# Performance work log

Measured on AMD Instinct MI355X. Metric: run time of the kernel, lower is better.

## Reference

```python
import jax, jax.numpy as jnp
import numpy as np

B, T, D, H = 128, 512, 64, 256  # batch, n_target, input_size, hidden_size

def setup_inputs() -> dict:
    key = jax.random.key(0)
    ks = jax.random.split(key, 12)
    sc_ih = 1.0 / np.sqrt(H)
    return {
        "x_input": jax.random.normal(ks[0], (B, T * D), dtype=jnp.float32),
        "h0": jax.random.normal(ks[1], (1, B, H), dtype=jnp.float32) * 0.1,
        "c0": jax.random.normal(ks[2], (1, B, H), dtype=jnp.float32) * 0.1,
        "W_ih": jax.random.normal(ks[3], (4 * H, D), dtype=jnp.float32) * sc_ih,
        "W_hh": jax.random.normal(ks[4], (4 * H, H), dtype=jnp.float32) * sc_ih,
        "b_ih": jax.random.normal(ks[5], (4 * H,), dtype=jnp.float32) * sc_ih,
        "b_hh": jax.random.normal(ks[6], (4 * H,), dtype=jnp.float32) * sc_ih,
        "f1_w": jax.random.normal(ks[7], (128, H), dtype=jnp.float32) * sc_ih,
        "f1_b": jax.random.normal(ks[8], (128,), dtype=jnp.float32) * sc_ih,
        "f2_w": jax.random.normal(ks[9], (128, H), dtype=jnp.float32) * sc_ih,
        "f2_b": jax.random.normal(ks[10], (128,), dtype=jnp.float32) * sc_ih,
        "long": 10,
    }

def reference(x_input, h0, c0, W_ih, W_hh, b_ih, b_hh, f1_w, f1_b, f2_w, f2_b, long):
    b = x_input.shape[0]
    d = W_ih.shape[1]
    state = x_input.reshape(b, -1, d)            # (B, T, D)
    t = state.shape[1]
    h_prev, c_prev = h0[0], c0[0]                # (B, H) shared initial state for every step
    # All single-step LSTM calls are independent -> one batched GEMM over (B, T)
    gates = (jnp.einsum('btd,gd->btg', state, W_ih) + b_ih
             + (h_prev @ W_hh.T + b_hh)[:, None, :])         # (B, T, 4H)
    i_g, f_g, g_g, o_g = jnp.split(gates, 4, axis=-1)        # torch gate order: i, f, g, o
    i_g = jax.nn.sigmoid(i_g); f_g = jax.nn.sigmoid(f_g)
    g_g = jnp.tanh(g_g);       o_g = jax.nn.sigmoid(o_g)
    c_all = f_g * c_prev[:, None, :] + i_g * g_g             # (B, T, H)
    h_all = o_g * jnp.tanh(c_all)
    # original loop starts at i=1, so step 0 keeps zero hidden/cell
    mask = (jnp.arange(t) > 0).astype(x_input.dtype)[None, :, None]
    h_all = h_all * mask
    c_all = c_all * mask
    w0 = state[:, :, 0] / long                               # (B, T)
    w1 = state[:, :, 1]
    def agg(v):
        a = jnp.einsum('bth,kh->btk', v, f1_w) + f1_b        # f1 per step
        bb = jnp.einsum('bth,kh->btk', v, f2_w) + f2_b       # f2 per step
        first = jnp.einsum('btk,bt->bk', a, w0)              # weighted sum over t
        second = jnp.einsum('btk,bt->bk', bb, w1)
        return jnp.concatenate([first, second], axis=-1)[None]  # (1, B, 256)
    return (agg(h_all), agg(c_all))
```

## Files before the change

### kernel.cpp

```cpp
#include <hip/hip_runtime.h>

#define BDIM 128
#define TDIM 512
#define DDIM 64
#define HDIM 256
#define BH   (BDIM * HDIM)
#define HH_OFF (4 * BH)

typedef short s16x8 __attribute__((ext_vector_type(8)));
typedef float f32x4 __attribute__((ext_vector_type(4)));

#if __has_builtin(__builtin_amdgcn_exp2f)
#define EXP2(x) __builtin_amdgcn_exp2f(x)
#else
#define EXP2(x) exp2f(x)
#endif
#define L2E 1.44269504f

__device__ __forceinline__ float rcpf(float x) { return __builtin_amdgcn_rcpf(x); }

__device__ __forceinline__ short f2bf(float f) {
  __bf16 b = (__bf16)f;
  return __builtin_bit_cast(short, b);
}

__device__ __forceinline__ s16x8 pack_bf8(float4 lo, float4 hi) {
  s16x8 v;
  v[0] = f2bf(lo.x); v[1] = f2bf(lo.y); v[2] = f2bf(lo.z); v[3] = f2bf(lo.w);
  v[4] = f2bf(hi.x); v[5] = f2bf(hi.y); v[6] = f2bf(hi.z); v[7] = f2bf(hi.w);
  return v;
}

__device__ __forceinline__ s16x8 pack_bf8s(float4 lo, float4 hi, float s) {
  s16x8 v;
  v[0] = f2bf(lo.x*s); v[1] = f2bf(lo.y*s); v[2] = f2bf(lo.z*s); v[3] = f2bf(lo.w*s);
  v[4] = f2bf(hi.x*s); v[5] = f2bf(hi.y*s); v[6] = f2bf(hi.z*s); v[7] = f2bf(hi.w*s);
  return v;
}

__global__ __launch_bounds__(256) void hh_mfma_kernel(
    const float* __restrict__ h0, const float* __restrict__ Whh,
    const float* __restrict__ bih, const float* __restrict__ bhh,
    float* __restrict__ hh)
{
  const int bt   = blockIdx.x;
  const int nt   = blockIdx.y;
  const int tid  = threadIdx.x;
  const int wave = tid >> 6;
  const int lane = tid & 63;
  const int col  = lane & 15;
  const int kg   = lane >> 4;
  const int b0   = bt * 16;
  const int colw = nt * 64 + wave * 16 + col;

  const float bias = bih[colw] + bhh[colw];

  const float* arow = h0  + (size_t)(b0 + col) * HDIM + kg * 8;
  const float* brow = Whh + (size_t)colw * HDIM + kg * 8;

  f32x4 acc = {0.f, 0.f, 0.f, 0.f};
  #pragma unroll
  for (int s = 0; s < 8; ++s) {
    float4 a0 = *(const float4*)(arow + s * 32);
    float4 a1 = *(const float4*)(arow + s * 32 + 4);
    float4 q0 = *(const float4*)(brow + s * 32);
    float4 q1 = *(const float4*)(brow + s * 32 + 4);
    acc = __builtin_amdgcn_mfma_f32_16x16x32_bf16(
        pack_bf8(a0, a1), pack_bf8(q0, q1), acc, 0, 0, 0);
  }

  #pragma unroll
  for (int r = 0; r < 4; ++r) {
    const int m = kg * 4 + r;
    hh[(size_t)(b0 + m) * 1024 + colw] = acc[r] + bias;
  }
}

__global__ __launch_bounds__(512, 4) void fused_lstm(
    const float* __restrict__ x, const float* __restrict__ c0,
    const float* __restrict__ Wih, const int* __restrict__ longp,
    float* __restrict__ sbuf)
{
  const int b    = blockIdx.x;
  const int hcq  = blockIdx.y;
  const int tid  = threadIdx.x;
  const int wave = tid >> 6;
  const int lane = tid & 63;
  const int col  = lane & 15;
  const int kg   = lane >> 4;
  const int hp   = wave & 1;
  const int tq   = wave >> 1;
  const int h    = hcq * 32 + hp * 16 + col;

  __shared__ float red[8 * 64];

  const float* hh = sbuf + HH_OFF;
  const float* xb = x + (size_t)b * (TDIM * DDIM);
  const float inv_long = 1.0f / (float)(*longp);

  const float SC[4] = {L2E, L2E, 2.f * L2E, L2E};
  float hhv[4];
  #pragma unroll
  for (int g = 0; g < 4; ++g)
    hhv[g] = hh[(size_t)b * 1024 + g * HDIM + h] * SC[g];
  const float cprev = c0[b * HDIM + h];

  s16x8 wf[4][2];
  #pragma unroll
  for (int g = 0; g < 4; ++g) {
    const float4* wrow = (const float4*)(Wih + (size_t)(g * HDIM + h) * DDIM);
    #pragma unroll
    for (int ks = 0; ks < 2; ++ks)
      wf[g][ks] = pack_bf8s(wrow[kg * 2 + ks * 8], wrow[kg * 2 + ks * 8 + 1], SC[g]);
  }

  const int t0w = tq * 128;
  const float* arow = xb + (size_t)(t0w + col) * DDIM + kg * 8;

  float4 nxt0 = *(const float4*)(arow + 0);
  float4 nxt1 = *(const float4*)(arow + 4);
  float4 nxt2 = *(const float4*)(arow + 32);
  float4 nxt3 = *(const float4*)(arow + 36);
  s16x8 a0 = pack_bf8(nxt0, nxt1);
  s16x8 a1 = pack_bf8(nxt2, nxt3);
  float w0c = nxt0.x, w1c = nxt0.y;
  if (tq == 0 && lane == 0) { w0c = 0.f; w1c = 0.f; }

  float s0h = 0.f, s1h = 0.f, s0c = 0.f, s1c = 0.f;

  for (int tb = 0; tb < 128; tb += 16) {
    const bool has_next = (tb + 16) < 128;
    if (has_next) {
      const float* p = arow + (size_t)(tb + 16) * DDIM;
      nxt0 = *(const float4*)(p + 0);
      nxt1 = *(const float4*)(p + 4);
      nxt2 = *(const float4*)(p + 32);
      nxt3 = *(const float4*)(p + 36);
    }

    f32x4 acc[4];
    #pragma unroll
    for (int g = 0; g < 4; ++g) {
      f32x4 zc = {hhv[g], hhv[g], hhv[g], hhv[g]};
      zc = __builtin_amdgcn_mfma_f32_16x16x32_bf16(a0, wf[g][0], zc, 0, 0, 0);
      zc = __builtin_amdgcn_mfma_f32_16x16x32_bf16(a1, wf[g][1], zc, 0, 0, 0);
      acc[g] = zc;
    }

    #pragma unroll
    for (int r = 0; r < 4; ++r) {
      float wx = __shfl(w0c, kg * 4 + r, 64);
      float wy = __shfl(w1c, kg * 4 + r, 64);
      float ig = rcpf(1.f + EXP2(-acc[0][r]));
      float fg = rcpf(1.f + EXP2(-acc[1][r]));
      float gg = fmaf(-2.f, rcpf(EXP2(acc[2][r]) + 1.f), 1.f);
      float og = rcpf(1.f + EXP2(-acc[3][r]));
      float cc = fmaf(fg, cprev, ig * gg);
      float th = fmaf(-2.f, rcpf(EXP2(cc * (2.f * L2E)) + 1.f), 1.f);
      float hv = og * th;
      s0h = fmaf(hv, wx, s0h); s1h = fmaf(hv, wy, s1h);
      s0c = fmaf(cc, wx, s0c); s1c = fmaf(cc, wy, s1c);
    }

    if (has_next) {
      a0 = pack_bf8(nxt0, nxt1);
      a1 = pack_bf8(nxt2, nxt3);
      w0c = nxt0.x; w1c = nxt0.y;
    }
  }

  s0h += __shfl_xor(s0h, 16, 64); s0h += __shfl_xor(s0h, 32, 64);
  s1h += __shfl_xor(s1h, 16, 64); s1h += __shfl_xor(s1h, 32, 64);
  s0c += __shfl_xor(s0c, 16, 64); s0c += __shfl_xor(s0c, 32, 64);
  s1c += __shfl_xor(s1c, 16, 64); s1c += __shfl_xor(s1c, 32, 64);

  if (kg == 0) {
    red[wave * 64 +  0 + col] = s0h * inv_long;
    red[wave * 64 + 16 + col] = s1h;
    red[wave * 64 + 32 + col] = s0c * inv_long;
    red[wave * 64 + 48 + col] = s1c;
  }
  __syncthreads();

  if (tid < 128) {
    const int hp2 = tid >> 6;
    const int q   = (tid >> 4) & 3;
    const int cc2 = tid & 15;
    const int o   = q * 16 + cc2;
    float s = red[(0 + hp2) * 64 + o] + red[(2 + hp2) * 64 + o] +
              red[(4 + hp2) * 64 + o] + red[(6 + hp2) * 64 + o];
    const int h2 = hcq * 32 + hp2 * 16 + cc2;
    sbuf[(size_t)q * BH + b * HDIM + h2] = s;
  }
}

__global__ __launch_bounds__(256) void out_kernel(
    const float* __restrict__ x, const float* __restrict__ f1w,
    const float* __restrict__ f1b, const float* __restrict__ f2w,
    const float* __restrict__ f2b, const int* __restrict__ longp,
    const float* __restrict__ sbuf, float* __restrict__ out)
{
  const int b = blockIdx.x, tid = threadIdx.x;
  __shared__ float s0h[256], s1h[256], s0c[256], s1c[256];
  __shared__ float wsum[8];
  const float* xb = x + (size_t)b * (TDIM * DDIM);

  s0h[tid] = sbuf[(size_t)0 * BH + b * HDIM + tid];
  s1h[tid] = sbuf[(size_t)1 * BH + b * HDIM + tid];
  s0c[tid] = sbuf[(size_t)2 * BH + b * HDIM + tid];
  s1c[tid] = sbuf[(size_t)3 * BH + b * HDIM + tid];

  float w0p = 0.f, w1p = 0.f;
  for (int t = tid; t < TDIM; t += 256) {
    float2 v = *(const float2*)(xb + (size_t)t * DDIM);
    w0p += v.x; w1p += v.y;
  }
  #pragma unroll
  for (int off = 1; off < 64; off <<= 1) {
    w0p += __shfl_xor(w0p, off, 64);
    w1p += __shfl_xor(w1p, off, 64);
  }
  if ((tid & 63) == 0) { wsum[tid >> 6] = w0p; wsum[4 + (tid >> 6)] = w1p; }
  __syncthreads();

  const float inv_long = 1.0f / (float)(*longp);
  const float W0 = (wsum[0] + wsum[1] + wsum[2] + wsum[3]) * inv_long;
  const float W1 = (wsum[4] + wsum[5] + wsum[6] + wsum[7]);

  float rh, rc;
  if (tid < 128) {
    const float4* wr = (const float4*)(f1w + (size_t)tid * HDIM);
    float ah = 0.f, ac = 0.f;
    #pragma unroll 8
    for (int k = 0; k < HDIM / 4; ++k) {
      float4 w = wr[k];
      ah += w.x * s0h[4*k] + w.y * s0h[4*k+1] + w.z * s0h[4*k+2] + w.w * s0h[4*k+3];
      ac += w.x * s0c[4*k] + w.y * s0c[4*k+1] + w.z * s0c[4*k+2] + w.w * s0c[4*k+3];
    }
    const float bb = f1b[tid];
    rh = ah + bb * W0;
    rc = ac + bb * W0;
  } else {
    const int k0 = tid - 128;
    const float4* wr = (const float4*)(f2w + (size_t)k0 * HDIM);
    float ah = 0.f, ac = 0.f;
    #pragma unroll 8
    for (int k = 0; k < HDIM / 4; ++k) {
      float4 w = wr[k];
      ah += w.x * s1h[4*k] + w.y * s1h[4*k+1] + w.z * s1h[4*k+2] + w.w * s1h[4*k+3];
      ac += w.x * s1c[4*k] + w.y * s1c[4*k+1] + w.z * s1c[4*k+2] + w.w * s1c[4*k+3];
    }
    const float bb = f2b[k0];
    rh = ah + bb * W1;
    rc = ac + bb * W1;
  }
  out[b * HDIM + tid] = rh;
  out[BDIM * HDIM + b * HDIM + tid] = rc;
}

extern "C" void kernel_launch(void* const* d_in, const int* in_sizes, int n_in,
                              void* d_out, int out_size, void* d_ws, size_t ws_size,
                              hipStream_t stream) {
  const float* x   = (const float*)d_in[0];
  const float* h0  = (const float*)d_in[1];
  const float* c0  = (const float*)d_in[2];
  const float* Wih = (const float*)d_in[3];
  const float* Whh = (const float*)d_in[4];
  const float* bih = (const float*)d_in[5];
  const float* bhh = (const float*)d_in[6];
  const float* f1w = (const float*)d_in[7];
  const float* f1b = (const float*)d_in[8];
  const float* f2w = (const float*)d_in[9];
  const float* f2b = (const float*)d_in[10];
  const int*  longp = (const int*)d_in[11];
  float* out  = (float*)d_out;
  float* sbuf = (float*)d_ws;

  dim3 gh(8, 16);
  hh_mfma_kernel<<<gh, 256, 0, stream>>>(h0, Whh, bih, bhh, sbuf + HH_OFF);
  dim3 g1(BDIM, 8);
  fused_lstm<<<g1, 512, 0, stream>>>(x, c0, Wih, longp, sbuf);
  out_kernel<<<BDIM, 256, 0, stream>>>(x, f1w, f1b, f2w, f2b, longp, sbuf, out);
}
```

Baseline: 66.36 us.

## Transpose MFMA operands so time runs along lanes and stage weights in LDS

Swaps the MFMA A/B operands so each lane's four accumulator rows cover four hidden units at a fixed time step, instead of four time steps at a fixed hidden unit. The per-step weights w0/w1 are staged once in LDS and read into registers up front, which removes the per-element __shfl calls from the inner loop. In exchange, per-lane state grows to 4 cprev and hh values plus 16 partial sums, and the final reduction needs 16 shuffle rounds over 16 lanes instead of 2 per sum. An extra __syncthreads and higher register pressure are added, which can lower occupancy.

```diff
diff --git a/kernel.cpp b/kernel.cpp
--- a/kernel.cpp
+++ b/kernel.cpp
@@ -90,31 +90,51 @@
   const int kg   = lane >> 4;
   const int hp   = wave & 1;
   const int tq   = wave >> 1;
-  const int h    = hcq * 32 + hp * 16 + col;
-
+  const int hbase = hcq * 32 + hp * 16;
+
+  __shared__ float2 ws01[TDIM];
   __shared__ float red[8 * 64];
 
   const float* hh = sbuf + HH_OFF;
   const float* xb = x + (size_t)b * (TDIM * DDIM);
   const float inv_long = 1.0f / (float)(*longp);
 
+  {
+    const float2 v = *(const float2*)(xb + (size_t)tid * DDIM);
+    ws01[tid] = (tid == 0) ? make_float2(0.f, 0.f) : v;
+  }
+  __syncthreads();
+
+  const int t0w = tq * 128;
+
+  float w0r[8], w1r[8];
+  #pragma unroll
+  for (int i = 0; i < 8; ++i) {
+    float2 v = ws01[t0w + i * 16 + col];
+    w0r[i] = v.x; w1r[i] = v.y;
+  }
+
   const float SC[4] = {L2E, L2E, 2.f * L2E, L2E};
-  float hhv[4];
-  #pragma unroll
-  for (int g = 0; g < 4; ++g)
-    hhv[g] = hh[(size_t)b * 1024 + g * HDIM + h] * SC[g];
-  const float cprev = c0[b * HDIM + h];
+  f32x4 hhv4[4];
+  float cprev[4];
+  #pragma unroll
+  for (int r = 0; r < 4; ++r) {
+    const int h = hbase + kg * 4 + r;
+    cprev[r] = c0[b * HDIM + h];
+    #pragma unroll
+    for (int g = 0; g < 4; ++g)
+      hhv4[g][r] = hh[(size_t)b * 1024 + g * HDIM + h] * SC[g];
+  }
 
   s16x8 wf[4][2];
   #pragma unroll
   for (int g = 0; g < 4; ++g) {
-    const float4* wrow = (const float4*)(Wih + (size_t)(g * HDIM + h) * DDIM);
+    const float4* wrow = (const float4*)(Wih + (size_t)(g * HDIM + hbase + col) * DDIM);
     #pragma unroll
     for (int ks = 0; ks < 2; ++ks)
       wf[g][ks] = pack_bf8s(wrow[kg * 2 + ks * 8], wrow[kg * 2 + ks * 8 + 1], SC[g]);
   }
 
-  const int t0w = tq * 128;
   const float* arow = xb + (size_t)(t0w + col) * DDIM + kg * 8;
 
   float4 nxt0 = *(const float4*)(arow + 0);
@@ -123,15 +143,15 @@
   float4 nxt3 = *(const float4*)(arow + 36);
   s16x8 a0 = pack_bf8(nxt0, nxt1);
   s16x8 a1 = pack_bf8(nxt2, nxt3);
-  float w0c = nxt0.x, w1c = nxt0.y;
-  if (tq == 0 && lane == 0) { w0c = 0.f; w1c = 0.f; }
-
-  float s0h = 0.f, s1h = 0.f, s0c = 0.f, s1c = 0.f;
-
-  for (int tb = 0; tb < 128; tb += 16) {
-    const bool has_next = (tb + 16) < 128;
+
+  float s0h[4] = {0,0,0,0}, s1h[4] = {0,0,0,0};
+  float s0c[4] = {0,0,0,0}, s1c[4] = {0,0,0,0};
+
+  #pragma unroll
+  for (int i = 0; i < 8; ++i) {
+    const bool has_next = (i + 1) < 8;
     if (has_next) {
-      const float* p = arow + (size_t)(tb + 16) * DDIM;
+      const float* p = arow + (size_t)((i + 1) * 16) * DDIM;
       nxt0 = *(const float4*)(p + 0);
       nxt1 = *(const float4*)(p + 4);
       nxt2 = *(const float4*)(p + 32);
@@ -141,44 +161,52 @@
     f32x4 acc[4];
     #pragma unroll
     for (int g = 0; g < 4; ++g) {
-      f32x4 zc = {hhv[g], hhv[g], hhv[g], hhv[g]};
-      zc = __builtin_amdgcn_mfma_f32_16x16x32_bf16(a0, wf[g][0], zc, 0, 0, 0);
-      zc = __builtin_amdgcn_mfma_f32_16x16x32_bf16(a1, wf[g][1], zc, 0, 0, 0);
+      f32x4 zc = hhv4[g];
+      zc = __builtin_amdgcn_mfma_f32_16x16x32_bf16(wf[g][0], a0, zc, 0, 0, 0);
+      zc = __builtin_amdgcn_mfma_f32_16x16x32_bf16(wf[g][1], a1, zc, 0, 0, 0);
       acc[g] = zc;
     }
 
+    const float wx = w0r[i], wy = w1r[i];
     #pragma unroll
     for (int r = 0; r < 4; ++r) {
-      float wx = __shfl(w0c, kg * 4 + r, 64);
-      float wy = __shfl(w1c, kg * 4 + r, 64);
       float ig = rcpf(1.f + EXP2(-acc[0][r]));
       float fg = rcpf(1.f + EXP2(-acc[1][r]));
       float gg = fmaf(-2.f, rcpf(EXP2(acc[2][r]) + 1.f), 1.f);
       float og = rcpf(1.f + EXP2(-acc[3][r]));
-      float cc = fmaf(fg, cprev, ig * gg);
+      float cc = fmaf(fg, cprev[r], ig * gg);
       float th = fmaf(-2.f, rcpf(EXP2(cc * (2.f * L2E)) + 1.f), 1.f);
       float hv = og * th;
-      s0h = fmaf(hv, wx, s0h); s1h = fmaf(hv, wy, s1h);
-      s0c = fmaf(cc, wx, s0c); s1c = fmaf(cc, wy, s1c);
+      s0h[r] = fmaf(hv, wx, s0h[r]); s1h[r] = fmaf(hv, wy, s1h[r]);
+      s0c[r] = fmaf(cc, wx, s0c[r]); s1c[r] = fmaf(cc, wy, s1c[r]);
     }
 
     if (has_next) {
       a0 = pack_bf8(nxt0, nxt1);
       a1 = pack_bf8(nxt2, nxt3);
-      w0c = nxt0.x; w1c = nxt0.y;
-    }
-  }
-
-  s0h += __shfl_xor(s0h, 16, 64); s0h += __shfl_xor(s0h, 32, 64);
-  s1h += __shfl_xor(s1h, 16, 64); s1h += __shfl_xor(s1h, 32, 64);
-  s0c += __shfl_xor(s0c, 16, 64); s0c += __shfl_xor(s0c, 32, 64);
-  s1c += __shfl_xor(s1c, 16, 64); s1c += __shfl_xor(s1c, 32, 64);
-
-  if (kg == 0) {
-    red[wave * 64 +  0 + col] = s0h * inv_long;
-    red[wave * 64 + 16 + col] = s1h;
-    red[wave * 64 + 32 + col] = s0c * inv_long;
-    red[wave * 64 + 48 + col] = s1c;
+    }
+  }
+
+  #pragma unroll
+  for (int r = 0; r < 4; ++r) {
+    #pragma unroll
+    for (int off = 1; off < 16; off <<= 1) {
+      s0h[r] += __shfl_xor(s0h[r], off, 64);
+      s1h[r] += __shfl_xor(s1h[r], off, 64);
+      s0c[r] += __shfl_xor(s0c[r], off, 64);
+      s1c[r] += __shfl_xor(s1c[r], off, 64);
+    }
+  }
+
+  if (col == 0) {
+    #pragma unroll
+    for (int r = 0; r < 4; ++r) {
+      const int hl = kg * 4 + r;
+      red[wave * 64 +  0 + hl] = s0h[r] * inv_long;
+      red[wave * 64 + 16 + hl] = s1h[r];
+      red[wave * 64 + 32 + hl] = s0c[r] * inv_long;
+      red[wave * 64 + 48 + hl] = s1c[r];
+    }
   }
   __syncthreads();
 
```

After: 71.12 us. 1.07x slower.

## Move per-batch weight sums into hh kernel and use MFMA for output projection

Applied to the files above, without the earlier changes.

The per-batch sums of x[:, :, 0] and x[:, :, 1] move out of the final kernel into an extra row of blocks in the hh kernel, which writes them to workspace. The output projection becomes a bf16 MFMA GEMM over an 8x8 grid of blocks instead of 128 blocks of scalar FP32 dot products. This shortens the tail kernel's critical path and spreads its work over more blocks, at the cost of bf16 rounding on the reduced sums and the f1/f2 weights.

```diff
diff --git a/kernel.cpp b/kernel.cpp
--- a/kernel.cpp
+++ b/kernel.cpp
@@ -4,8 +4,9 @@
 #define TDIM 512
 #define DDIM 64
 #define HDIM 256
-#define BH   (BDIM * HDIM)
-#define HH_OFF (4 * BH)
+#define BH    (BDIM * HDIM)
+#define W_OFF (4 * BH)
+#define HH_OFF (W_OFF + 256)
 
 typedef short s16x8 __attribute__((ext_vector_type(8)));
 typedef float f32x4 __attribute__((ext_vector_type(4)));
@@ -41,7 +42,8 @@
 __global__ __launch_bounds__(256) void hh_mfma_kernel(
     const float* __restrict__ h0, const float* __restrict__ Whh,
     const float* __restrict__ bih, const float* __restrict__ bhh,
-    float* __restrict__ hh)
+    const float* __restrict__ x, const int* __restrict__ longp,
+    float* __restrict__ sbuf)
 {
   const int bt   = blockIdx.x;
   const int nt   = blockIdx.y;
@@ -51,8 +53,30 @@
   const int col  = lane & 15;
   const int kg   = lane >> 4;
   const int b0   = bt * 16;
+
+  if (nt == 16) {
+    const int bl = tid >> 4, part = tid & 15;
+    const int b = b0 + bl;
+    const float* xb = x + (size_t)b * (TDIM * DDIM);
+    const float inv_long = 1.0f / (float)(*longp);
+    float sa = 0.f, sb = 0.f;
+    for (int t = part; t < TDIM; t += 16) {
+      float2 v = *(const float2*)(xb + (size_t)t * DDIM);
+      sa += v.x; sb += v.y;
+    }
+    #pragma unroll
+    for (int off = 1; off < 16; off <<= 1) {
+      sa += __shfl_xor(sa, off, 64);
+      sb += __shfl_xor(sb, off, 64);
+    }
+    if (part == 0) {
+      sbuf[W_OFF + b * 2 + 0] = sa * inv_long;
+      sbuf[W_OFF + b * 2 + 1] = sb;
+    }
+    return;
+  }
+
   const int colw = nt * 64 + wave * 16 + col;
-
   const float bias = bih[colw] + bhh[colw];
 
   const float* arow = h0  + (size_t)(b0 + col) * HDIM + kg * 8;
@@ -69,6 +93,7 @@
         pack_bf8(a0, a1), pack_bf8(q0, q1), acc, 0, 0, 0);
   }
 
+  float* hh = sbuf + HH_OFF;
   #pragma unroll
   for (int r = 0; r < 4; ++r) {
     const int m = kg * 4 + r;
@@ -194,68 +219,49 @@
   }
 }
 
-__global__ __launch_bounds__(256) void out_kernel(
-    const float* __restrict__ x, const float* __restrict__ f1w,
-    const float* __restrict__ f1b, const float* __restrict__ f2w,
-    const float* __restrict__ f2b, const int* __restrict__ longp,
+__global__ __launch_bounds__(256) void out_mfma_kernel(
+    const float* __restrict__ f1w, const float* __restrict__ f1b,
+    const float* __restrict__ f2w, const float* __restrict__ f2b,
     const float* __restrict__ sbuf, float* __restrict__ out)
 {
-  const int b = blockIdx.x, tid = threadIdx.x;
-  __shared__ float s0h[256], s1h[256], s0c[256], s1c[256];
-  __shared__ float wsum[8];
-  const float* xb = x + (size_t)b * (TDIM * DDIM);
-
-  s0h[tid] = sbuf[(size_t)0 * BH + b * HDIM + tid];
-  s1h[tid] = sbuf[(size_t)1 * BH + b * HDIM + tid];
-  s0c[tid] = sbuf[(size_t)2 * BH + b * HDIM + tid];
-  s1c[tid] = sbuf[(size_t)3 * BH + b * HDIM + tid];
-
-  float w0p = 0.f, w1p = 0.f;
-  for (int t = tid; t < TDIM; t += 256) {
-    float2 v = *(const float2*)(xb + (size_t)t * DDIM);
-    w0p += v.x; w1p += v.y;
-  }
-  #pragma unroll
-  for (int off = 1; off < 64; off <<= 1) {
-    w0p += __shfl_xor(w0p, off, 64);
-    w1p += __shfl_xor(w1p, off, 64);
-  }
-  if ((tid & 63) == 0) { wsum[tid >> 6] = w0p; wsum[4 + (tid >> 6)] = w1p; }
-  __syncthreads();
-
-  const float inv_long = 1.0f / (float)(*longp);
-  const float W0 = (wsum[0] + wsum[1] + wsum[2] + wsum[3]) * inv_long;
-  const float W1 = (wsum[4] + wsum[5] + wsum[6] + wsum[7]);
-
-  float rh, rc;
-  if (tid < 128) {
-    const float4* wr = (const float4*)(f1w + (size_t)tid * HDIM);
-    float ah = 0.f, ac = 0.f;
-    #pragma unroll 8
-    for (int k = 0; k < HDIM / 4; ++k) {
-      float4 w = wr[k];
-      ah += w.x * s0h[4*k] + w.y * s0h[4*k+1] + w.z * s0h[4*k+2] + w.w * s0h[4*k+3];
-      ac += w.x * s0c[4*k] + w.y * s0c[4*k+1] + w.z * s0c[4*k+2] + w.w * s0c[4*k+3];
-    }
-    const float bb = f1b[tid];
-    rh = ah + bb * W0;
-    rc = ac + bb * W0;
-  } else {
-    const int k0 = tid - 128;
-    const float4* wr = (const float4*)(f2w + (size_t)k0 * HDIM);
-    float ah = 0.f, ac = 0.f;
-    #pragma unroll 8
-    for (int k = 0; k < HDIM / 4; ++k) {
-      float4 w = wr[k];
-      ah += w.x * s1h[4*k] + w.y * s1h[4*k+1] + w.z * s1h[4*k+2] + w.w * s1h[4*k+3];
-      ac += w.x * s1c[4*k] + w.y * s1c[4*k+1] + w.z * s1c[4*k+2] + w.w * s1c[4*k+3];
-    }
-    const float bb = f2b[k0];
-    rh = ah + bb * W1;
-    rc = ac + bb * W1;
-  }
-  out[b * HDIM + tid] = rh;
-  out[BDIM * HDIM + b * HDIM + tid] = rc;
+  const int bt   = blockIdx.x;
+  const int kt   = blockIdx.y;
+  const int tid  = threadIdx.x;
+  const int wave = tid >> 6;
+  const int lane = tid & 63;
+  const int col  = lane & 15;
+  const int kg   = lane >> 4;
+  const int b0   = bt * 16;
+  const int k0   = kt * 16;
+
+  const int q        = (wave == 0) ? 0 : (wave == 1) ? 2 : (wave == 2) ? 1 : 3;
+  const float* Wm    = (wave < 2) ? f1w : f2w;
+  const float* bv    = (wave < 2) ? f1b : f2b;
+  const int   kout   = (wave < 2) ? k0 : (128 + k0);
+  const int   opl    = (wave & 1);
+  const int   wsel   = (wave < 2) ? 0 : 1;
+
+  const float* arow = sbuf + (size_t)q * BH + (size_t)(b0 + col) * HDIM + kg * 8;
+  const float* brow = Wm + (size_t)(k0 + col) * HDIM + kg * 8;
+
+  f32x4 acc = {0.f, 0.f, 0.f, 0.f};
+  #pragma unroll
+  for (int s = 0; s < 8; ++s) {
+    float4 a0 = *(const float4*)(arow + s * 32);
+    float4 a1 = *(const float4*)(arow + s * 32 + 4);
+    float4 q0 = *(const float4*)(brow + s * 32);
+    float4 q1 = *(const float4*)(brow + s * 32 + 4);
+    acc = __builtin_amdgcn_mfma_f32_16x16x32_bf16(
+        pack_bf8(a0, a1), pack_bf8(q0, q1), acc, 0, 0, 0);
+  }
+
+  const float bw = bv[k0 + col];
+  #pragma unroll
+  for (int r = 0; r < 4; ++r) {
+    const int b = b0 + kg * 4 + r;
+    const float Wv = sbuf[W_OFF + b * 2 + wsel];
+    out[(size_t)opl * BH + (size_t)b * HDIM + kout + col] = acc[r] + bw * Wv;
+  }
 }
 
 extern "C" void kernel_launch(void* const* d_in, const int* in_sizes, int n_in,
@@ -276,9 +282,10 @@
   float* out  = (float*)d_out;
   float* sbuf = (float*)d_ws;
 
-  dim3 gh(8, 16);
-  hh_mfma_kernel<<<gh, 256, 0, stream>>>(h0, Whh, bih, bhh, sbuf + HH_OFF);
+  dim3 gh(8, 17);
+  hh_mfma_kernel<<<gh, 256, 0, stream>>>(h0, Whh, bih, bhh, x, longp, sbuf);
   dim3 g1(BDIM, 8);
   fused_lstm<<<g1, 512, 0, stream>>>(x, c0, Wih, longp, sbuf);
-  out_kernel<<<BDIM, 256, 0, stream>>>(x, f1w, f1b, f2w, f2b, longp, sbuf, out);
-}
+  dim3 go(8, 8);
+  out_mfma_kernel<<<go, 256, 0, stream>>>(f1w, f1b, f2w, f2b, sbuf, out);
+}
```

Measured after the change: 66.38 us. No clear change (+0.0%).
